# Performance work log

Measured on AMD Instinct MI355X. Metric: run time of the kernel, lower is better.

The kernel has to match this reference:

```python
import jax, jax.numpy as jnp
import numpy as np
import math

B, S, D, H = 4, 2048, 1024, 16
HD = D // H
MASKED_BIAS = -10000.0

def setup_inputs() -> dict:
    key = jax.random.key(0)
    k1, k2, k3, k4, k5 = jax.random.split(key, 5)
    scale = 0.02
    return {
        "hidden_states": jax.random.normal(k1, (B, S, D), dtype=jnp.float32),
        "w_attn": jax.random.normal(k2, (D, 3 * D), dtype=jnp.float32) * scale,
        "b_attn": jnp.zeros((3 * D,), dtype=jnp.float32),
        "w_proj": jax.random.normal(k3, (D, D), dtype=jnp.float32) * scale,
        "b_proj": jnp.zeros((D,), dtype=jnp.float32),
    }

def reference(hidden_states, w_attn, b_attn, w_proj, b_proj):
    b, s, d = hidden_states.shape
    qkv = hidden_states @ w_attn + b_attn                      # [B,S,3D]
    q, k, v = jnp.split(qkv, 3, axis=-1)
    # split heads -> [B,H,S,HD]
    def split_heads(x):
        return x.reshape(b, s, H, HD).transpose(0, 2, 1, 3)
    q, k, v = split_heads(q), split_heads(k), split_heads(v)
    scores = jnp.einsum("bhqd,bhkd->bhqk", q, k) / math.sqrt(HD)
    causal = jnp.tril(jnp.ones((s, s), dtype=bool))
    scores = jnp.where(causal[None, None], scores, jnp.float32(MASKED_BIAS))
    probs = jax.nn.softmax(scores, axis=-1)
    ctx = jnp.einsum("bhqk,bhkd->bhqd", probs, v)
    ctx = ctx.transpose(0, 2, 1, 3).reshape(b, s, d)           # merge heads
    return ctx @ w_proj + b_proj
```

## Files before the change

### kernel.cpp

```cpp
#include <hip/hip_runtime.h>

typedef unsigned short u16;
typedef __attribute__((ext_vector_type(8))) short short8;
typedef __attribute__((ext_vector_type(4))) float f32x4;
typedef __attribute__((ext_vector_type(4))) unsigned u32x4;

#define Bq 4
#define Sq 2048
#define Dq 1024
#define Hq 16
#define HDq 64
#define BSq 8192

#define QSCALE 0.18033688011112042f

__device__ __forceinline__ u16 f2bf(float f) {
  unsigned u = __builtin_bit_cast(unsigned, f);
  unsigned r = u + 0x7fffu + ((u >> 16) & 1u);
  return (u16)(r >> 16);
}

__device__ __forceinline__ unsigned pk2(float a, float b) {
  unsigned ua = __builtin_bit_cast(unsigned, a) + 0x8000u;
  unsigned ub = __builtin_bit_cast(unsigned, b) + 0x8000u;
  return __builtin_amdgcn_perm(ub, ua, 0x07060302u);
}

__device__ __forceinline__ unsigned cvtpk(float a, float b) {
  unsigned r;
  asm("v_cvt_pk_bf16_f32 %0, %1, %2" : "=v"(r) : "v"(a), "v"(b));
  return r;
}

__device__ __forceinline__ void gl_lds16(const u16* g, u16* l) {
  __builtin_amdgcn_global_load_lds((const __attribute__((address_space(1))) unsigned int*)g,
                                   (__attribute__((address_space(3))) unsigned int*)l, 16, 0, 0);
}

#define WAITV4()  asm volatile("s_waitcnt vmcnt(4)" ::: "memory")
#define WAITV0()  asm volatile("s_waitcnt vmcnt(0)" ::: "memory")
#define PHASE_BAR() do { __builtin_amdgcn_sched_barrier(0); \
                         __builtin_amdgcn_s_barrier();      \
                         __builtin_amdgcn_sched_barrier(0); } while (0)

__device__ __forceinline__ int kperm(int kk) {
  return ((kk & 0x10) << 1) | ((kk & 0x0C) << 1) | ((kk & 0x20) >> 3) | (kk & 3);
}

__global__ void cvt_kernel(const float* __restrict__ in, u16* __restrict__ out, int n4) {
  int i = blockIdx.x * blockDim.x + threadIdx.x;
  if (i >= n4) return;
  float4 v = reinterpret_cast<const float4*>(in)[i];
  ushort4 o;
  o.x = f2bf(v.x); o.y = f2bf(v.y); o.z = f2bf(v.z); o.w = f2bf(v.w);
  reinterpret_cast<ushort4*>(out)[i] = o;
}

__global__ void transpose_cvt(const float* __restrict__ in, u16* __restrict__ out, int R, int C) {
  __shared__ float tile[32][33];
  int c0 = blockIdx.x * 32, r0 = blockIdx.y * 32;
  for (int i = threadIdx.y; i < 32; i += 8)
    tile[i][threadIdx.x] = in[(size_t)(r0 + i) * C + c0 + threadIdx.x];
  __syncthreads();
  for (int i = threadIdx.y; i < 32; i += 8)
    out[(size_t)(c0 + i) * R + r0 + threadIdx.x] = f2bf(tile[threadIdx.x][i]);
}

template<int EPI>
__global__ __launch_bounds__(256)
void gemm_bt(const u16* __restrict__ A, const u16* __restrict__ Bt,
             const float* __restrict__ bias,
             u16* __restrict__ Qb, u16* __restrict__ Kb, u16* __restrict__ Vt,
             float* __restrict__ Out, int Kdim) {
  __shared__ __align__(16) u16 As[3][128 * 32];
  __shared__ __align__(16) u16 Bs[3][128 * 32];
  int tid = threadIdx.x;
  int lane = tid & 63, wid = tid >> 6;
  int wr = wid >> 1, wc = wid & 1;
  constexpr int NX = (EPI == 0) ? 24 : 8;
  constexpr int NWG = NX * 64;
  int orig = (int)blockIdx.x + NX * (int)blockIdx.y;
  int swz = (orig & 7) * (NWG >> 3) + (orig >> 3);
  int m0 = (swz / NX) * 128, n0 = (swz % NX) * 128;
  int l15 = lane & 15, g = lane >> 4;
  f32x4 acc[4][4] = {};
  int srow = tid >> 2;
  int scol = (((tid & 3) ^ ((tid >> 3) & 3)) * 8);
  int crd = (g ^ ((l15 >> 1) & 3)) * 8;

  const u16* a0p = &A[(size_t)(m0 + srow) * Kdim + scol];
  const u16* a1p = &A[(size_t)(m0 + 64 + srow) * Kdim + scol];
  const u16* b0p = &Bt[(size_t)(n0 + srow) * Kdim + scol];
  const u16* b1p = &Bt[(size_t)(n0 + 64 + srow) * Kdim + scol];

  gl_lds16(a0p,      &As[0][wid * 512]);
  gl_lds16(a1p,      &As[0][2048 + wid * 512]);
  gl_lds16(b0p,      &Bs[0][wid * 512]);
  gl_lds16(b1p,      &Bs[0][2048 + wid * 512]);
  gl_lds16(a0p + 32, &As[1][wid * 512]);
  gl_lds16(a1p + 32, &As[1][2048 + wid * 512]);
  gl_lds16(b0p + 32, &Bs[1][wid * 512]);
  gl_lds16(b1p + 32, &Bs[1][2048 + wid * 512]);
  WAITV4();
  PHASE_BAR();

  int nk = Kdim >> 5;
  int cur = 0;
  for (int t = 0; t < nk; ++t) {
    bool more = (t + 2) < nk;
    if (more) {
      int nxt = cur + 2; if (nxt >= 3) nxt -= 3;
      int ko = (t + 2) << 5;
      gl_lds16(a0p + ko, &As[nxt][wid * 512]);
      gl_lds16(a1p + ko, &As[nxt][2048 + wid * 512]);
      gl_lds16(b0p + ko, &Bs[nxt][wid * 512]);
      gl_lds16(b1p + ko, &Bs[nxt][2048 + wid * 512]);
    }
    short8 af[4], bfr[4];
#pragma unroll
    for (int m = 0; m < 4; ++m)
      af[m] = *reinterpret_cast<const short8*>(&As[cur][(wr * 64 + m * 16 + l15) * 32 + crd]);
#pragma unroll
    for (int n = 0; n < 4; ++n)
      bfr[n] = *reinterpret_cast<const short8*>(&Bs[cur][(wc * 64 + n * 16 + l15) * 32 + crd]);
    __builtin_amdgcn_s_setprio(1);
#pragma unroll
    for (int m = 0; m < 4; ++m)
#pragma unroll
      for (int n = 0; n < 4; ++n)
        acc[m][n] = __builtin_amdgcn_mfma_f32_16x16x32_bf16(af[m], bfr[n], acc[m][n], 0, 0, 0);
    __builtin_amdgcn_s_setprio(0);
    if (more) WAITV4();
    else      WAITV0();
    PHASE_BAR();
    cur = cur + 1; if (cur >= 3) cur -= 3;
  }

  int bb = (m0 + wr * 64) >> 11;
  int sb = (m0 + wr * 64) & 2047;

  if (EPI == 1) {
#pragma unroll
    for (int m = 0; m < 4; ++m)
#pragma unroll
      for (int n = 0; n < 4; ++n) {
        int gcol = n0 + wc * 64 + n * 16 + l15;
        float bv = bias[gcol];
#pragma unroll
        for (int r = 0; r < 4; ++r) {
          int grow = m0 + wr * 64 + m * 16 + g * 4 + r;
          Out[(size_t)grow * 1024 + gcol] = acc[m][n][r] + bv;
        }
      }
  } else if (n0 < 1024) {
#pragma unroll
    for (int n = 0; n < 4; ++n) {
      int col = n0 + wc * 64 + n * 16 + l15;
      int hh = col >> 6, d = col & 63;
      float bv = bias[col];
      u16* qb = &Qb[(((size_t)(bb * 16 + hh) * 2048 + sb) << 6) + d];
#pragma unroll
      for (int m = 0; m < 4; ++m)
#pragma unroll
        for (int r = 0; r < 4; ++r)
          qb[(size_t)(m * 16 + g * 4 + r) << 6] = f2bf((acc[m][n][r] + bv) * QSCALE);
    }
  } else if (n0 < 2048) {
#pragma unroll
    for (int n = 0; n < 4; ++n) {
      int col = n0 - 1024 + wc * 64 + n * 16 + l15;
      int hh = col >> 6, d = col & 63;
      float bv = bias[1024 + col];
      u16* kb = &Kb[(((size_t)(bb * 16 + hh) * 2048 + sb) << 6) + d];
#pragma unroll
      for (int m = 0; m < 4; ++m)
#pragma unroll
        for (int r = 0; r < 4; ++r)
          kb[(size_t)(m * 16 + g * 4 + r) << 6] = f2bf(acc[m][n][r] + bv);
    }
  } else {
#pragma unroll
    for (int n = 0; n < 4; ++n) {
      int cc = n0 - 2048 + wc * 64 + n * 16 + l15;
      int hh = cc >> 6, d = cc & 63;
      float bv = bias[2048 + cc];
      u16* dst = &Vt[((size_t)(bb * 16 + hh) * 64 + d) * 2048 + sb];
      u32x4 lo, hi;
      lo[0] = pk2(acc[0][n][0] + bv, acc[0][n][1] + bv);
      lo[1] = pk2(acc[0][n][2] + bv, acc[0][n][3] + bv);
      lo[2] = pk2(acc[2][n][0] + bv, acc[2][n][1] + bv);
      lo[3] = pk2(acc[2][n][2] + bv, acc[2][n][3] + bv);
      hi[0] = pk2(acc[1][n][0] + bv, acc[1][n][1] + bv);
      hi[1] = pk2(acc[1][n][2] + bv, acc[1][n][3] + bv);
      hi[2] = pk2(acc[3][n][0] + bv, acc[3][n][1] + bv);
      hi[3] = pk2(acc[3][n][2] + bv, acc[3][n][3] + bv);
      *reinterpret_cast<u32x4*>(dst + g * 8) = lo;
      *reinterpret_cast<u32x4*>(dst + 32 + g * 8) = hi;
    }
  }
}

__global__ __launch_bounds__(256, 2)
void attn_kernel(const u16* __restrict__ Qb, const u16* __restrict__ Kb,
                 const u16* __restrict__ Vt, u16* __restrict__ Ctx) {
  __shared__ __align__(16) u16 lds[2][2][8][512];
  int tid = threadIdx.x, lane = tid & 63, w = tid >> 6;
  int l15 = lane & 15, g = lane >> 4;
  int bh = blockIdx.y;
  const u16* Qh = Qb + (size_t)bh * Sq * HDq;
  const u16* Kh = Kb + (size_t)bh * Sq * HDq;
  const u16* Vh = Vt + (size_t)bh * HDq * Sq;
  int b = bh >> 4, h = bh & 15;

  int tileA = 31 - (int)blockIdx.x, tileB = (int)blockIdx.x;
  int nkA = tileA + 1;
  int ntot = nkA + tileB + 1;

  const u16* ksrc = Kh + (size_t)(16 * w + l15) * 64 + 8 * g;
  const u16* vsrc = Vh + (size_t)(16 * w + l15) * Sq + 8 * g;
  const u16* kpre = ksrc + 4096;
  const u16* vpre = vsrc + 64;

  int tile = tileA;
  int qbase = tileA * 64 + w * 16;

  short8 qf[2];
  qf[0] = *reinterpret_cast<const short8*>(&Qh[(size_t)(qbase + l15) * 64 + 8 * g]);
  qf[1] = *reinterpret_cast<const short8*>(&Qh[(size_t)(qbase + l15) * 64 + 32 + 8 * g]);

  u16 onebits = (l15 == 0) ? (u16)0x3F80 : (u16)0;
  short8 vones;
#pragma unroll
  for (int i = 0; i < 8; ++i) vones[i] = (short)onebits;

  f32x4 acc[4] = {};
  f32x4 acc_l = {};
  float m_r = -INFINITY;

  gl_lds16(ksrc,      &lds[0][0][2 * w][0]);
  gl_lds16(ksrc + 32, &lds[0][0][2 * w + 1][0]);
  gl_lds16(vsrc,      &lds[0][1][2 * w][0]);
  gl_lds16(vsrc + 32, &lds[0][1][2 * w + 1][0]);
  __syncthreads();
  int cur = 0;
  int kb = 0;

#pragma unroll 1
  for (int it = 0; it < ntot; ++it) {
    bool lastA = (it == nkA - 1);
    int k0 = kb << 6;

    if (it + 1 < ntot) {
      gl_lds16(kpre,      &lds[cur ^ 1][0][2 * w][0]);
      gl_lds16(kpre + 32, &lds[cur ^ 1][0][2 * w + 1][0]);
      gl_lds16(vpre,      &lds[cur ^ 1][1][2 * w][0]);
      gl_lds16(vpre + 32, &lds[cur ^ 1][1][2 * w + 1][0]);
      if (it == nkA - 2) { kpre = ksrc; vpre = vsrc; }
      else               { kpre += 4096; vpre += 64; }
    }

    short8 kf[4][2], vbf[4][2];
#pragma unroll
    for (int j = 0; j < 4; ++j) {
      kf[j][0] = *reinterpret_cast<const short8*>(&lds[cur][0][2 * j][lane * 8]);
      kf[j][1] = *reinterpret_cast<const short8*>(&lds[cur][0][2 * j + 1][lane * 8]);
    }
#pragma unroll
    for (int n = 0; n < 4; ++n) {
      vbf[n][0] = *reinterpret_cast<const short8*>(&lds[cur][1][2 * n][lane * 8]);
      vbf[n][1] = *reinterpret_cast<const short8*>(&lds[cur][1][2 * n + 1][lane * 8]);
    }

    f32x4 sj[4];
    __builtin_amdgcn_s_setprio(1);
#pragma unroll
    for (int j = 0; j < 4; ++j) {
      f32x4 z = {};
      z = __builtin_amdgcn_mfma_f32_16x16x32_bf16(kf[j][0], qf[0], z, 0, 0, 0);
      z = __builtin_amdgcn_mfma_f32_16x16x32_bf16(kf[j][1], qf[1], z, 0, 0, 0);
      sj[j] = z;
    }
    __builtin_amdgcn_s_setprio(0);

    if (kb == tile) {
      int q = qbase + l15;
#pragma unroll
      for (int j = 0; j < 4; ++j)
#pragma unroll
        for (int r = 0; r < 4; ++r)
          if (k0 + 16 * j + 4 * g + r > q) sj[j][r] = -1e30f;
    }

    float a0 = fmaxf(fmaxf(sj[0][0], sj[0][1]), sj[0][2]);
    float a1 = fmaxf(fmaxf(sj[0][3], sj[1][0]), sj[1][1]);
    float a2 = fmaxf(fmaxf(sj[1][2], sj[1][3]), sj[2][0]);
    float a3 = fmaxf(fmaxf(sj[2][1], sj[2][2]), sj[2][3]);
    float a4 = fmaxf(fmaxf(sj[3][0], sj[3][1]), sj[3][2]);
    float mx = fmaxf(fmaxf(fmaxf(a0, a1), a2), fmaxf(fmaxf(a3, a4), sj[3][3]));
    mx = fmaxf(mx, __shfl_xor(mx, 16));
    mx = fmaxf(mx, __shfl_xor(mx, 32));

    float mn = m_r;
    if (!__all(mx - mn <= 8.0f)) {
      float mnew = fmaxf(mn, mx);
      float scn = exp2f(mn - mnew);
      float scr[4];
#pragma unroll
      for (int r = 0; r < 4; ++r) scr[r] = __shfl(scn, 4 * g + r);
#pragma unroll
      for (int n = 0; n < 4; ++n)
#pragma unroll
        for (int r = 0; r < 4; ++r) acc[n][r] *= scr[r];
#pragma unroll
      for (int r = 0; r < 4; ++r) acc_l[r] *= scr[r];
      m_r = mnew;
      mn = mnew;
    }

    float p[4][4];
#pragma unroll
    for (int j = 0; j < 4; ++j)
#pragma unroll
      for (int r = 0; r < 4; ++r)
        p[j][r] = exp2f(sj[j][r] - mn);

    u32x4 w0, w1;
    w0[0] = cvtpk(p[0][0], p[0][1]); w0[1] = cvtpk(p[0][2], p[0][3]);
    w0[2] = cvtpk(p[2][0], p[2][1]); w0[3] = cvtpk(p[2][2], p[2][3]);
    w1[0] = cvtpk(p[1][0], p[1][1]); w1[1] = cvtpk(p[1][2], p[1][3]);
    w1[2] = cvtpk(p[3][0], p[3][1]); w1[3] = cvtpk(p[3][2], p[3][3]);
    short8 pa0 = __builtin_bit_cast(short8, w0);
    short8 pa1 = __builtin_bit_cast(short8, w1);
    __builtin_amdgcn_s_setprio(1);
#pragma unroll
    for (int n = 0; n < 4; ++n) {
      acc[n] = __builtin_amdgcn_mfma_f32_16x16x32_bf16(pa0, vbf[n][0], acc[n], 0, 0, 0);
      acc[n] = __builtin_amdgcn_mfma_f32_16x16x32_bf16(pa1, vbf[n][1], acc[n], 0, 0, 0);
    }
    acc_l = __builtin_amdgcn_mfma_f32_16x16x32_bf16(pa0, vones, acc_l, 0, 0, 0);
    acc_l = __builtin_amdgcn_mfma_f32_16x16x32_bf16(pa1, vones, acc_l, 0, 0, 0);
    __builtin_amdgcn_s_setprio(0);

    kb++;
    if (lastA) {
      float lf[4];
#pragma unroll
      for (int r = 0; r < 4; ++r) lf[r] = __shfl(acc_l[r], 16 * g);
#pragma unroll
      for (int r = 0; r < 4; ++r) {
        float inv = 1.0f / lf[r];
        int row = qbase + 4 * g + r;
        size_t obase = ((size_t)(b * Sq + row)) * Dq + h * 64;
#pragma unroll
        for (int n = 0; n < 4; ++n)
          Ctx[obase + 16 * n + l15] = f2bf(acc[n][r] * inv);
      }
      qbase = tileB * 64 + w * 16;
      tile = tileB;
      kb = 0;
      qf[0] = *reinterpret_cast<const short8*>(&Qh[(size_t)(qbase + l15) * 64 + 8 * g]);
      qf[1] = *reinterpret_cast<const short8*>(&Qh[(size_t)(qbase + l15) * 64 + 32 + 8 * g]);
#pragma unroll
      for (int n = 0; n < 4; ++n) acc[n] = f32x4{};
      acc_l = f32x4{};
      m_r = -INFINITY;
    }

    __syncthreads();
    cur ^= 1;
  }

  {
    float lf[4];
#pragma unroll
    for (int r = 0; r < 4; ++r) lf[r] = __shfl(acc_l[r], 16 * g);
#pragma unroll
    for (int r = 0; r < 4; ++r) {
      float inv = 1.0f / lf[r];
      int row = qbase + 4 * g + r;
      size_t obase = ((size_t)(b * Sq + row)) * Dq + h * 64;
#pragma unroll
      for (int n = 0; n < 4; ++n)
        Ctx[obase + 16 * n + l15] = f2bf(acc[n][r] * inv);
    }
  }
}

extern "C" void kernel_launch(void* const* d_in, const int* in_sizes, int n_in,
                              void* d_out, int out_size, void* d_ws, size_t ws_size,
                              hipStream_t stream) {
  const float* X  = (const float*)d_in[0];
  const float* Wa = (const float*)d_in[1];
  const float* Ba = (const float*)d_in[2];
  const float* Wp = (const float*)d_in[3];
  const float* Bp = (const float*)d_in[4];
  float* Out = (float*)d_out;

  u16* ws  = (u16*)d_ws;
  u16* Xb  = ws;
  u16* WaT = Xb  + (size_t)BSq * Dq;
  u16* WpT = WaT + (size_t)3 * Dq * Dq;
  u16* Qb  = WpT + (size_t)Dq * Dq;
  u16* Kb  = Qb  + (size_t)Bq * Hq * Sq * HDq;
  u16* Vt  = Kb  + (size_t)Bq * Hq * Sq * HDq;
  u16* Ctx = Vt  + (size_t)Bq * Hq * Sq * HDq;

  cvt_kernel<<<(BSq * Dq / 4 + 255) / 256, 256, 0, stream>>>(X, Xb, BSq * Dq / 4);
  transpose_cvt<<<dim3(3 * Dq / 32, Dq / 32), dim3(32, 8), 0, stream>>>(Wa, WaT, Dq, 3 * Dq);
  transpose_cvt<<<dim3(Dq / 32, Dq / 32), dim3(32, 8), 0, stream>>>(Wp, WpT, Dq, Dq);
  gemm_bt<0><<<dim3(3 * Dq / 128, BSq / 128), 256, 0, stream>>>(Xb, WaT, Ba, Qb, Kb, Vt, nullptr, Dq);
  attn_kernel<<<dim3(16, Bq * Hq), 256, 0, stream>>>(Qb, Kb, Vt, Ctx);
  gemm_bt<1><<<dim3(Dq / 128, BSq / 128), 256, 0, stream>>>(Ctx, WpT, Bp, nullptr, nullptr, nullptr, Out, Dq);
}
```

Baseline: 196.9 us.

## Enlarge GEMM tiles to 256x256 with 512-thread blocks

Both GEMMs (QKV projection and output projection) move from 128x128 tiles with 4 waves to 256x256 tiles with 8 waves. Each wave now computes a 128x64 sub-tile with 8x4 MFMA accumulators, and the LDS staging and epilogues are rewritten to match. The goal is more operand reuse per LDS load and less global traffic per FLOP. In exchange, register and LDS use per block go up sharply (about 96KB LDS per block), which likely limits residency to one block per CU. The grids also shrink a lot: the output-projection GEMM drops to 128 blocks, which may leave many CUs idle.

```diff
diff --git a/kernel.cpp b/kernel.cpp
--- a/kernel.cpp
+++ b/kernel.cpp
@@ -67,40 +67,42 @@
 }
 
 template<int EPI>
-__global__ __launch_bounds__(256)
+__global__ __launch_bounds__(512, 2)
 void gemm_bt(const u16* __restrict__ A, const u16* __restrict__ Bt,
              const float* __restrict__ bias,
              u16* __restrict__ Qb, u16* __restrict__ Kb, u16* __restrict__ Vt,
              float* __restrict__ Out, int Kdim) {
-  __shared__ __align__(16) u16 As[3][128 * 32];
-  __shared__ __align__(16) u16 Bs[3][128 * 32];
+  __shared__ __align__(16) u16 As[3][256 * 32];
+  __shared__ __align__(16) u16 Bs[3][256 * 32];
   int tid = threadIdx.x;
-  int lane = tid & 63, wid = tid >> 6;
-  int wr = wid >> 1, wc = wid & 1;
-  constexpr int NX = (EPI == 0) ? 24 : 8;
-  constexpr int NWG = NX * 64;
-  int orig = (int)blockIdx.x + NX * (int)blockIdx.y;
+  int lane = tid & 63;
+  int wid = tid >> 6;
+  int wrM = wid >> 2, wcN = wid & 3;
+  constexpr int NXT = (EPI == 0) ? 12 : 4;
+  constexpr int NWG = NXT * 32;
+  int orig = (int)blockIdx.x + NXT * (int)blockIdx.y;
   int swz = (orig & 7) * (NWG >> 3) + (orig >> 3);
-  int m0 = (swz / NX) * 128, n0 = (swz % NX) * 128;
+  int m0 = (swz / NXT) * 256, n0 = (swz % NXT) * 256;
   int l15 = lane & 15, g = lane >> 4;
-  f32x4 acc[4][4] = {};
-  int srow = tid >> 2;
-  int scol = (((tid & 3) ^ ((tid >> 3) & 3)) * 8);
+  f32x4 acc[8][4] = {};
+
+  int f1 = 512 + tid;
+  int r0s = tid >> 2, c0s = ((tid & 3) ^ ((r0s >> 1) & 3)) * 8;
+  int r1s = f1 >> 2,  c1s = ((f1 & 3) ^ ((r1s >> 1) & 3)) * 8;
+  const u16* aP0 = &A[(size_t)(m0 + r0s) * Kdim + c0s];
+  const u16* aP1 = &A[(size_t)(m0 + r1s) * Kdim + c1s];
+  const u16* bP0 = &Bt[(size_t)(n0 + r0s) * Kdim + c0s];
+  const u16* bP1 = &Bt[(size_t)(n0 + r1s) * Kdim + c1s];
   int crd = (g ^ ((l15 >> 1) & 3)) * 8;
 
-  const u16* a0p = &A[(size_t)(m0 + srow) * Kdim + scol];
-  const u16* a1p = &A[(size_t)(m0 + 64 + srow) * Kdim + scol];
-  const u16* b0p = &Bt[(size_t)(n0 + srow) * Kdim + scol];
-  const u16* b1p = &Bt[(size_t)(n0 + 64 + srow) * Kdim + scol];
-
-  gl_lds16(a0p,      &As[0][wid * 512]);
-  gl_lds16(a1p,      &As[0][2048 + wid * 512]);
-  gl_lds16(b0p,      &Bs[0][wid * 512]);
-  gl_lds16(b1p,      &Bs[0][2048 + wid * 512]);
-  gl_lds16(a0p + 32, &As[1][wid * 512]);
-  gl_lds16(a1p + 32, &As[1][2048 + wid * 512]);
-  gl_lds16(b0p + 32, &Bs[1][wid * 512]);
-  gl_lds16(b1p + 32, &Bs[1][2048 + wid * 512]);
+  gl_lds16(aP0,      &As[0][tid * 8]);
+  gl_lds16(aP1,      &As[0][f1 * 8]);
+  gl_lds16(bP0,      &Bs[0][tid * 8]);
+  gl_lds16(bP1,      &Bs[0][f1 * 8]);
+  gl_lds16(aP0 + 32, &As[1][tid * 8]);
+  gl_lds16(aP1 + 32, &As[1][f1 * 8]);
+  gl_lds16(bP0 + 32, &Bs[1][tid * 8]);
+  gl_lds16(bP1 + 32, &Bs[1][f1 * 8]);
   WAITV4();
   PHASE_BAR();
 
@@ -111,91 +113,98 @@
     if (more) {
       int nxt = cur + 2; if (nxt >= 3) nxt -= 3;
       int ko = (t + 2) << 5;
-      gl_lds16(a0p + ko, &As[nxt][wid * 512]);
-      gl_lds16(a1p + ko, &As[nxt][2048 + wid * 512]);
-      gl_lds16(b0p + ko, &Bs[nxt][wid * 512]);
-      gl_lds16(b1p + ko, &Bs[nxt][2048 + wid * 512]);
-    }
-    short8 af[4], bfr[4];
-#pragma unroll
-    for (int m = 0; m < 4; ++m)
-      af[m] = *reinterpret_cast<const short8*>(&As[cur][(wr * 64 + m * 16 + l15) * 32 + crd]);
+      gl_lds16(aP0 + ko, &As[nxt][tid * 8]);
+      gl_lds16(aP1 + ko, &As[nxt][f1 * 8]);
+      gl_lds16(bP0 + ko, &Bs[nxt][tid * 8]);
+      gl_lds16(bP1 + ko, &Bs[nxt][f1 * 8]);
+    }
+    short8 bf[4];
 #pragma unroll
     for (int n = 0; n < 4; ++n)
-      bfr[n] = *reinterpret_cast<const short8*>(&Bs[cur][(wc * 64 + n * 16 + l15) * 32 + crd]);
-    __builtin_amdgcn_s_setprio(1);
-#pragma unroll
-    for (int m = 0; m < 4; ++m)
+      bf[n] = *reinterpret_cast<const short8*>(&Bs[cur][(wcN * 64 + n * 16 + l15) * 32 + crd]);
+#pragma unroll
+    for (int qq = 0; qq < 4; ++qq) {
+      short8 af0 = *reinterpret_cast<const short8*>(&As[cur][(wrM * 128 + (2 * qq) * 16 + l15) * 32 + crd]);
+      short8 af1 = *reinterpret_cast<const short8*>(&As[cur][(wrM * 128 + (2 * qq + 1) * 16 + l15) * 32 + crd]);
+      __builtin_amdgcn_s_setprio(1);
 #pragma unroll
       for (int n = 0; n < 4; ++n)
-        acc[m][n] = __builtin_amdgcn_mfma_f32_16x16x32_bf16(af[m], bfr[n], acc[m][n], 0, 0, 0);
-    __builtin_amdgcn_s_setprio(0);
+        acc[2 * qq][n] = __builtin_amdgcn_mfma_f32_16x16x32_bf16(af0, bf[n], acc[2 * qq][n], 0, 0, 0);
+#pragma unroll
+      for (int n = 0; n < 4; ++n)
+        acc[2 * qq + 1][n] = __builtin_amdgcn_mfma_f32_16x16x32_bf16(af1, bf[n], acc[2 * qq + 1][n], 0, 0, 0);
+      __builtin_amdgcn_s_setprio(0);
+    }
     if (more) WAITV4();
     else      WAITV0();
     PHASE_BAR();
     cur = cur + 1; if (cur >= 3) cur -= 3;
   }
 
-  int bb = (m0 + wr * 64) >> 11;
-  int sb = (m0 + wr * 64) & 2047;
+  int bb = (m0 + wrM * 128) >> 11;
+  int sb = (m0 + wrM * 128) & 2047;
+  int colb = n0 + wcN * 64;
 
   if (EPI == 1) {
 #pragma unroll
-    for (int m = 0; m < 4; ++m)
-#pragma unroll
-      for (int n = 0; n < 4; ++n) {
-        int gcol = n0 + wc * 64 + n * 16 + l15;
-        float bv = bias[gcol];
-#pragma unroll
-        for (int r = 0; r < 4; ++r) {
-          int grow = m0 + wr * 64 + m * 16 + g * 4 + r;
-          Out[(size_t)grow * 1024 + gcol] = acc[m][n][r] + bv;
-        }
-      }
+    for (int n = 0; n < 4; ++n) {
+      int gcol = colb + n * 16 + l15;
+      float bv = bias[gcol];
+#pragma unroll
+      for (int m = 0; m < 8; ++m)
+#pragma unroll
+        for (int r = 0; r < 4; ++r)
+          Out[(size_t)(m0 + wrM * 128 + m * 16 + g * 4 + r) * 1024 + gcol] = acc[m][n][r] + bv;
+    }
   } else if (n0 < 1024) {
-#pragma unroll
-    for (int n = 0; n < 4; ++n) {
-      int col = n0 + wc * 64 + n * 16 + l15;
-      int hh = col >> 6, d = col & 63;
-      float bv = bias[col];
+    int hh = colb >> 6;
+#pragma unroll
+    for (int n = 0; n < 4; ++n) {
+      int d = n * 16 + l15;
+      float bv = bias[colb + d];
       u16* qb = &Qb[(((size_t)(bb * 16 + hh) * 2048 + sb) << 6) + d];
 #pragma unroll
-      for (int m = 0; m < 4; ++m)
+      for (int m = 0; m < 8; ++m)
 #pragma unroll
         for (int r = 0; r < 4; ++r)
           qb[(size_t)(m * 16 + g * 4 + r) << 6] = f2bf((acc[m][n][r] + bv) * QSCALE);
     }
   } else if (n0 < 2048) {
-#pragma unroll
-    for (int n = 0; n < 4; ++n) {
-      int col = n0 - 1024 + wc * 64 + n * 16 + l15;
-      int hh = col >> 6, d = col & 63;
-      float bv = bias[1024 + col];
+    int cb = colb - 1024;
+    int hh = cb >> 6;
+#pragma unroll
+    for (int n = 0; n < 4; ++n) {
+      int d = n * 16 + l15;
+      float bv = bias[1024 + cb + d];
       u16* kb = &Kb[(((size_t)(bb * 16 + hh) * 2048 + sb) << 6) + d];
 #pragma unroll
-      for (int m = 0; m < 4; ++m)
+      for (int m = 0; m < 8; ++m)
 #pragma unroll
         for (int r = 0; r < 4; ++r)
           kb[(size_t)(m * 16 + g * 4 + r) << 6] = f2bf(acc[m][n][r] + bv);
     }
   } else {
-#pragma unroll
-    for (int n = 0; n < 4; ++n) {
-      int cc = n0 - 2048 + wc * 64 + n * 16 + l15;
-      int hh = cc >> 6, d = cc & 63;
-      float bv = bias[2048 + cc];
+    int cb = colb - 2048;
+    int hh = cb >> 6;
+#pragma unroll
+    for (int n = 0; n < 4; ++n) {
+      int d = n * 16 + l15;
+      float bv = bias[2048 + cb + d];
       u16* dst = &Vt[((size_t)(bb * 16 + hh) * 64 + d) * 2048 + sb];
-      u32x4 lo, hi;
-      lo[0] = pk2(acc[0][n][0] + bv, acc[0][n][1] + bv);
-      lo[1] = pk2(acc[0][n][2] + bv, acc[0][n][3] + bv);
-      lo[2] = pk2(acc[2][n][0] + bv, acc[2][n][1] + bv);
-      lo[3] = pk2(acc[2][n][2] + bv, acc[2][n][3] + bv);
-      hi[0] = pk2(acc[1][n][0] + bv, acc[1][n][1] + bv);
-      hi[1] = pk2(acc[1][n][2] + bv, acc[1][n][3] + bv);
-      hi[2] = pk2(acc[3][n][0] + bv, acc[3][n][1] + bv);
-      hi[3] = pk2(acc[3][n][2] + bv, acc[3][n][3] + bv);
-      *reinterpret_cast<u32x4*>(dst + g * 8) = lo;
-      *reinterpret_cast<u32x4*>(dst + 32 + g * 8) = hi;
+#pragma unroll
+      for (int mg = 0; mg < 2; ++mg) {
+        u32x4 lo, hi;
+        lo[0] = pk2(acc[4 * mg + 0][n][0] + bv, acc[4 * mg + 0][n][1] + bv);
+        lo[1] = pk2(acc[4 * mg + 0][n][2] + bv, acc[4 * mg + 0][n][3] + bv);
+        lo[2] = pk2(acc[4 * mg + 2][n][0] + bv, acc[4 * mg + 2][n][1] + bv);
+        lo[3] = pk2(acc[4 * mg + 2][n][2] + bv, acc[4 * mg + 2][n][3] + bv);
+        hi[0] = pk2(acc[4 * mg + 1][n][0] + bv, acc[4 * mg + 1][n][1] + bv);
+        hi[1] = pk2(acc[4 * mg + 1][n][2] + bv, acc[4 * mg + 1][n][3] + bv);
+        hi[2] = pk2(acc[4 * mg + 3][n][0] + bv, acc[4 * mg + 3][n][1] + bv);
+        hi[3] = pk2(acc[4 * mg + 3][n][2] + bv, acc[4 * mg + 3][n][3] + bv);
+        *reinterpret_cast<u32x4*>(dst + mg * 64 + g * 8) = lo;
+        *reinterpret_cast<u32x4*>(dst + mg * 64 + 32 + g * 8) = hi;
+      }
     }
   }
 }
@@ -408,7 +417,7 @@
   cvt_kernel<<<(BSq * Dq / 4 + 255) / 256, 256, 0, stream>>>(X, Xb, BSq * Dq / 4);
   transpose_cvt<<<dim3(3 * Dq / 32, Dq / 32), dim3(32, 8), 0, stream>>>(Wa, WaT, Dq, 3 * Dq);
   transpose_cvt<<<dim3(Dq / 32, Dq / 32), dim3(32, 8), 0, stream>>>(Wp, WpT, Dq, Dq);
-  gemm_bt<0><<<dim3(3 * Dq / 128, BSq / 128), 256, 0, stream>>>(Xb, WaT, Ba, Qb, Kb, Vt, nullptr, Dq);
+  gemm_bt<0><<<dim3(12, 32), 512, 0, stream>>>(Xb, WaT, Ba, Qb, Kb, Vt, nullptr, Dq);
   attn_kernel<<<dim3(16, Bq * Hq), 256, 0, stream>>>(Qb, Kb, Vt, Ctx);
-  gemm_bt<1><<<dim3(Dq / 128, BSq / 128), 256, 0, stream>>>(Ctx, WpT, Bp, nullptr, nullptr, nullptr, Out, Dq);
-}
+  gemm_bt<1><<<dim3(4, 32), 512, 0, stream>>>(Ctx, WpT, Bp, nullptr, nullptr, nullptr, Out, Dq);
+}
```

Measured after the change: 226.5 us. +15.0%, slower.

## Double query rows per wave to reuse K/V tiles across two subtiles

Applied to the files above, without the earlier changes.

Each block now handles 128-row query tiles, with every wave processing two 16-row query subtiles against each loaded 64-key K/V tile. The grid is halved to 8 x 64 blocks, still paired with causal load balancing. This halves the K/V LDS traffic and global loads per query row. In exchange it adds register pressure from doubled accumulators and halves the block count, which may reduce occupancy and load balance on the GPU.

```diff
diff --git a/kernel.cpp b/kernel.cpp
--- a/kernel.cpp
+++ b/kernel.cpp
@@ -212,30 +212,32 @@
   const u16* Vh = Vt + (size_t)bh * HDq * Sq;
   int b = bh >> 4, h = bh & 15;
 
-  int tileA = 31 - (int)blockIdx.x, tileB = (int)blockIdx.x;
-  int nkA = tileA + 1;
-  int ntot = nkA + tileB + 1;
+  int tileA = 15 - (int)blockIdx.x, tileB = (int)blockIdx.x;
+  int nkA = 2 * tileA + 2;
+  int ntot = nkA + 2 * tileB + 2;
 
   const u16* ksrc = Kh + (size_t)(16 * w + l15) * 64 + 8 * g;
   const u16* vsrc = Vh + (size_t)(16 * w + l15) * Sq + 8 * g;
   const u16* kpre = ksrc + 4096;
   const u16* vpre = vsrc + 64;
 
-  int tile = tileA;
-  int qbase = tileA * 64 + w * 16;
-
-  short8 qf[2];
-  qf[0] = *reinterpret_cast<const short8*>(&Qh[(size_t)(qbase + l15) * 64 + 8 * g]);
-  qf[1] = *reinterpret_cast<const short8*>(&Qh[(size_t)(qbase + l15) * 64 + 32 + 8 * g]);
+  int qbase = tileA * 128 + w * 32;
+
+  short8 qf[2][2];
+#pragma unroll
+  for (int s = 0; s < 2; ++s)
+#pragma unroll
+    for (int hh = 0; hh < 2; ++hh)
+      qf[s][hh] = *reinterpret_cast<const short8*>(&Qh[(size_t)(qbase + 16 * s + l15) * 64 + 32 * hh + 8 * g]);
 
   u16 onebits = (l15 == 0) ? (u16)0x3F80 : (u16)0;
   short8 vones;
 #pragma unroll
   for (int i = 0; i < 8; ++i) vones[i] = (short)onebits;
 
-  f32x4 acc[4] = {};
-  f32x4 acc_l = {};
-  float m_r = -INFINITY;
+  f32x4 acc[2][4] = {};
+  f32x4 acc_l[2] = {};
+  float m_r[2] = {-INFINITY, -INFINITY};
 
   gl_lds16(ksrc,      &lds[0][0][2 * w][0]);
   gl_lds16(ksrc + 32, &lds[0][0][2 * w + 1][0]);
@@ -271,99 +273,110 @@
       vbf[n][1] = *reinterpret_cast<const short8*>(&lds[cur][1][2 * n + 1][lane * 8]);
     }
 
-    f32x4 sj[4];
-    __builtin_amdgcn_s_setprio(1);
-#pragma unroll
-    for (int j = 0; j < 4; ++j) {
-      f32x4 z = {};
-      z = __builtin_amdgcn_mfma_f32_16x16x32_bf16(kf[j][0], qf[0], z, 0, 0, 0);
-      z = __builtin_amdgcn_mfma_f32_16x16x32_bf16(kf[j][1], qf[1], z, 0, 0, 0);
-      sj[j] = z;
-    }
-    __builtin_amdgcn_s_setprio(0);
-
-    if (kb == tile) {
-      int q = qbase + l15;
+#pragma unroll
+    for (int s = 0; s < 2; ++s) {
+      int q0s = qbase + 16 * s;
+
+      f32x4 sj[4];
+      __builtin_amdgcn_s_setprio(1);
+#pragma unroll
+      for (int j = 0; j < 4; ++j) {
+        f32x4 z = {};
+        z = __builtin_amdgcn_mfma_f32_16x16x32_bf16(kf[j][0], qf[s][0], z, 0, 0, 0);
+        z = __builtin_amdgcn_mfma_f32_16x16x32_bf16(kf[j][1], qf[s][1], z, 0, 0, 0);
+        sj[j] = z;
+      }
+      __builtin_amdgcn_s_setprio(0);
+
+      if (k0 + 63 > q0s) {
+        int q = q0s + l15;
+#pragma unroll
+        for (int j = 0; j < 4; ++j)
+#pragma unroll
+          for (int r = 0; r < 4; ++r)
+            if (k0 + 16 * j + 4 * g + r > q) sj[j][r] = -1e30f;
+      }
+
+      float a0 = fmaxf(fmaxf(sj[0][0], sj[0][1]), sj[0][2]);
+      float a1 = fmaxf(fmaxf(sj[0][3], sj[1][0]), sj[1][1]);
+      float a2 = fmaxf(fmaxf(sj[1][2], sj[1][3]), sj[2][0]);
+      float a3 = fmaxf(fmaxf(sj[2][1], sj[2][2]), sj[2][3]);
+      float a4 = fmaxf(fmaxf(sj[3][0], sj[3][1]), sj[3][2]);
+      float mx = fmaxf(fmaxf(fmaxf(a0, a1), a2), fmaxf(fmaxf(a3, a4), sj[3][3]));
+      mx = fmaxf(mx, __shfl_xor(mx, 16));
+      mx = fmaxf(mx, __shfl_xor(mx, 32));
+
+      float mn = m_r[s];
+      if (!__all(mx - mn <= 8.0f)) {
+        float mnew = fmaxf(mn, mx);
+        float scn = exp2f(mn - mnew);
+        float scr[4];
+#pragma unroll
+        for (int r = 0; r < 4; ++r) scr[r] = __shfl(scn, 4 * g + r);
+#pragma unroll
+        for (int n = 0; n < 4; ++n)
+#pragma unroll
+          for (int r = 0; r < 4; ++r) acc[s][n][r] *= scr[r];
+#pragma unroll
+        for (int r = 0; r < 4; ++r) acc_l[s][r] *= scr[r];
+        m_r[s] = mnew;
+        mn = mnew;
+      }
+
+      float p[4][4];
 #pragma unroll
       for (int j = 0; j < 4; ++j)
 #pragma unroll
         for (int r = 0; r < 4; ++r)
-          if (k0 + 16 * j + 4 * g + r > q) sj[j][r] = -1e30f;
-    }
-
-    float a0 = fmaxf(fmaxf(sj[0][0], sj[0][1]), sj[0][2]);
-    float a1 = fmaxf(fmaxf(sj[0][3], sj[1][0]), sj[1][1]);
-    float a2 = fmaxf(fmaxf(sj[1][2], sj[1][3]), sj[2][0]);
-    float a3 = fmaxf(fmaxf(sj[2][1], sj[2][2]), sj[2][3]);
-    float a4 = fmaxf(fmaxf(sj[3][0], sj[3][1]), sj[3][2]);
-    float mx = fmaxf(fmaxf(fmaxf(a0, a1), a2), fmaxf(fmaxf(a3, a4), sj[3][3]));
-    mx = fmaxf(mx, __shfl_xor(mx, 16));
-    mx = fmaxf(mx, __shfl_xor(mx, 32));
-
-    float mn = m_r;
-    if (!__all(mx - mn <= 8.0f)) {
-      float mnew = fmaxf(mn, mx);
-      float scn = exp2f(mn - mnew);
-      float scr[4];
-#pragma unroll
-      for (int r = 0; r < 4; ++r) scr[r] = __shfl(scn, 4 * g + r);
-#pragma unroll
-      for (int n = 0; n < 4; ++n)
-#pragma unroll
-        for (int r = 0; r < 4; ++r) acc[n][r] *= scr[r];
-#pragma unroll
-      for (int r = 0; r < 4; ++r) acc_l[r] *= scr[r];
-      m_r = mnew;
-      mn = mnew;
-    }
-
-    float p[4][4];
-#pragma unroll
-    for (int j = 0; j < 4; ++j)
-#pragma unroll
-      for (int r = 0; r < 4; ++r)
-        p[j][r] = exp2f(sj[j][r] - mn);
-
-    u32x4 w0, w1;
-    w0[0] = cvtpk(p[0][0], p[0][1]); w0[1] = cvtpk(p[0][2], p[0][3]);
-    w0[2] = cvtpk(p[2][0], p[2][1]); w0[3] = cvtpk(p[2][2], p[2][3]);
-    w1[0] = cvtpk(p[1][0], p[1][1]); w1[1] = cvtpk(p[1][2], p[1][3]);
-    w1[2] = cvtpk(p[3][0], p[3][1]); w1[3] = cvtpk(p[3][2], p[3][3]);
-    short8 pa0 = __builtin_bit_cast(short8, w0);
-    short8 pa1 = __builtin_bit_cast(short8, w1);
-    __builtin_amdgcn_s_setprio(1);
-#pragma unroll
-    for (int n = 0; n < 4; ++n) {
-      acc[n] = __builtin_amdgcn_mfma_f32_16x16x32_bf16(pa0, vbf[n][0], acc[n], 0, 0, 0);
-      acc[n] = __builtin_amdgcn_mfma_f32_16x16x32_bf16(pa1, vbf[n][1], acc[n], 0, 0, 0);
-    }
-    acc_l = __builtin_amdgcn_mfma_f32_16x16x32_bf16(pa0, vones, acc_l, 0, 0, 0);
-    acc_l = __builtin_amdgcn_mfma_f32_16x16x32_bf16(pa1, vones, acc_l, 0, 0, 0);
-    __builtin_amdgcn_s_setprio(0);
+          p[j][r] = exp2f(sj[j][r] - mn);
+
+      u32x4 w0, w1;
+      w0[0] = cvtpk(p[0][0], p[0][1]); w0[1] = cvtpk(p[0][2], p[0][3]);
+      w0[2] = cvtpk(p[2][0], p[2][1]); w0[3] = cvtpk(p[2][2], p[2][3]);
+      w1[0] = cvtpk(p[1][0], p[1][1]); w1[1] = cvtpk(p[1][2], p[1][3]);
+      w1[2] = cvtpk(p[3][0], p[3][1]); w1[3] = cvtpk(p[3][2], p[3][3]);
+      short8 pa0 = __builtin_bit_cast(short8, w0);
+      short8 pa1 = __builtin_bit_cast(short8, w1);
+      __builtin_amdgcn_s_setprio(1);
+#pragma unroll
+      for (int n = 0; n < 4; ++n) {
+        acc[s][n] = __builtin_amdgcn_mfma_f32_16x16x32_bf16(pa0, vbf[n][0], acc[s][n], 0, 0, 0);
+        acc[s][n] = __builtin_amdgcn_mfma_f32_16x16x32_bf16(pa1, vbf[n][1], acc[s][n], 0, 0, 0);
+      }
+      acc_l[s] = __builtin_amdgcn_mfma_f32_16x16x32_bf16(pa0, vones, acc_l[s], 0, 0, 0);
+      acc_l[s] = __builtin_amdgcn_mfma_f32_16x16x32_bf16(pa1, vones, acc_l[s], 0, 0, 0);
+      __builtin_amdgcn_s_setprio(0);
+    }
 
     kb++;
     if (lastA) {
-      float lf[4];
-#pragma unroll
-      for (int r = 0; r < 4; ++r) lf[r] = __shfl(acc_l[r], 16 * g);
-#pragma unroll
-      for (int r = 0; r < 4; ++r) {
-        float inv = 1.0f / lf[r];
-        int row = qbase + 4 * g + r;
-        size_t obase = ((size_t)(b * Sq + row)) * Dq + h * 64;
-#pragma unroll
-        for (int n = 0; n < 4; ++n)
-          Ctx[obase + 16 * n + l15] = f2bf(acc[n][r] * inv);
-      }
-      qbase = tileB * 64 + w * 16;
-      tile = tileB;
+#pragma unroll
+      for (int s = 0; s < 2; ++s) {
+        float lf[4];
+#pragma unroll
+        for (int r = 0; r < 4; ++r) lf[r] = __shfl(acc_l[s][r], 16 * g);
+#pragma unroll
+        for (int r = 0; r < 4; ++r) {
+          float inv = 1.0f / lf[r];
+          int row = qbase + 16 * s + 4 * g + r;
+          size_t obase = ((size_t)(b * Sq + row)) * Dq + h * 64;
+#pragma unroll
+          for (int n = 0; n < 4; ++n)
+            Ctx[obase + 16 * n + l15] = f2bf(acc[s][n][r] * inv);
+        }
+      }
+      qbase = tileB * 128 + w * 32;
       kb = 0;
-      qf[0] = *reinterpret_cast<const short8*>(&Qh[(size_t)(qbase + l15) * 64 + 8 * g]);
-      qf[1] = *reinterpret_cast<const short8*>(&Qh[(size_t)(qbase + l15) * 64 + 32 + 8 * g]);
-#pragma unroll
-      for (int n = 0; n < 4; ++n) acc[n] = f32x4{};
-      acc_l = f32x4{};
-      m_r = -INFINITY;
+#pragma unroll
+      for (int s = 0; s < 2; ++s) {
+#pragma unroll
+        for (int hh = 0; hh < 2; ++hh)
+          qf[s][hh] = *reinterpret_cast<const short8*>(&Qh[(size_t)(qbase + 16 * s + l15) * 64 + 32 * hh + 8 * g]);
+#pragma unroll
+        for (int n = 0; n < 4; ++n) acc[s][n] = f32x4{};
+        acc_l[s] = f32x4{};
+        m_r[s] = -INFINITY;
+      }
     }
 
     __syncthreads();
@@ -371,17 +384,20 @@
   }
 
   {
-    float lf[4];
-#pragma unroll
-    for (int r = 0; r < 4; ++r) lf[r] = __shfl(acc_l[r], 16 * g);
-#pragma unroll
-    for (int r = 0; r < 4; ++r) {
-      float inv = 1.0f / lf[r];
-      int row = qbase + 4 * g + r;
-      size_t obase = ((size_t)(b * Sq + row)) * Dq + h * 64;
-#pragma unroll
-      for (int n = 0; n < 4; ++n)
-        Ctx[obase + 16 * n + l15] = f2bf(acc[n][r] * inv);
+#pragma unroll
+    for (int s = 0; s < 2; ++s) {
+      float lf[4];
+#pragma unroll
+      for (int r = 0; r < 4; ++r) lf[r] = __shfl(acc_l[s][r], 16 * g);
+#pragma unroll
+      for (int r = 0; r < 4; ++r) {
+        float inv = 1.0f / lf[r];
+        int row = qbase + 16 * s + 4 * g + r;
+        size_t obase = ((size_t)(b * Sq + row)) * Dq + h * 64;
+#pragma unroll
+        for (int n = 0; n < 4; ++n)
+          Ctx[obase + 16 * n + l15] = f2bf(acc[s][n][r] * inv);
+      }
     }
   }
 }
@@ -409,6 +425,6 @@
   transpose_cvt<<<dim3(3 * Dq / 32, Dq / 32), dim3(32, 8), 0, stream>>>(Wa, WaT, Dq, 3 * Dq);
   transpose_cvt<<<dim3(Dq / 32, Dq / 32), dim3(32, 8), 0, stream>>>(Wp, WpT, Dq, Dq);
   gemm_bt<0><<<dim3(3 * Dq / 128, BSq / 128), 256, 0, stream>>>(Xb, WaT, Ba, Qb, Kb, Vt, nullptr, Dq);
-  attn_kernel<<<dim3(16, Bq * Hq), 256, 0, stream>>>(Qb, Kb, Vt, Ctx);
+  attn_kernel<<<dim3(8, Bq * Hq), 256, 0, stream>>>(Qb, Kb, Vt, Ctx);
   gemm_bt<1><<<dim3(Dq / 128, BSq / 128), 256, 0, stream>>>(Ctx, WpT, Bp, nullptr, nullptr, nullptr, Out, Dq);
 }
```

Result: slower. 206.5 us (+4.8%).
